# Kernel tuning notes

Measured on AMD Instinct MI355X. Metric: run time of the kernel, lower is better.

Reference implementation:

```python
import jax, jax.numpy as jnp
import numpy as np

K = 16  # number of neighbors (self excluded), matches init k
NUM_CLASSES = 100


def setup_inputs() -> dict:
    key = jax.random.key(0)
    kx, ky = jax.random.split(key)
    N, D = 8192, 256
    x = jax.random.normal(kx, (N, D), dtype=jnp.float32)
    y = jax.random.randint(ky, (N,), 0, NUM_CLASSES, dtype=jnp.int64)
    return {"x": x, "y": y}


def _knn_loss(x, y):
    N = x.shape[0]
    k = min(K, N - 1)
    # Pairwise squared Euclidean distances via Gram trick: [N, N]
    sq_norms = jnp.sum(x * x, axis=1)
    sq = sq_norms[:, None] + sq_norms[None, :] - 2.0 * (x @ x.T)
    sq = jnp.maximum(sq, 0.0)
    eye = jnp.eye(N, dtype=bool)
    # Keep sqrt grad-safe on the (excluded) diagonal by placing a dummy 1.0 there.
    d = jnp.sqrt(jnp.where(eye, 1.0, sq))  # [N, N] Euclidean distances

    # k nearest neighbors excluding self (BallTree query k+1 then drop col 0).
    d_for_knn = jnp.where(eye, jnp.inf, d)
    _, nn_idx = jax.lax.top_k(-d_for_knn, k)  # [N, k] indices of smallest distances

    # distances = exp(-d); denominator sums over all j != i.
    exp_d = jnp.where(eye, 0.0, jnp.exp(-d))
    denom = jnp.sum(exp_d, axis=1)  # [N]

    # log(exp(-d_in) / denom_i) = -d_in - log(denom_i)
    nn_d = jnp.take_along_axis(d, nn_idx, axis=1)          # [N, k]
    log_p = -nn_d - jnp.log(denom)[:, None]                 # [N, k]

    # Only neighbors with matching label contribute; rows with none are skipped.
    match = (y[nn_idx] == y[:, None]).astype(x.dtype)       # [N, k]
    cnt = jnp.sum(match, axis=1)                            # [N]
    row_mean = jnp.where(cnt > 0, jnp.sum(log_p * match, axis=1) / jnp.maximum(cnt, 1.0), 0.0)
    return -jnp.sum(row_mean) / N


def reference(x, y):
    return _knn_loss(x, y)
```

## Files before the change

kernel.cpp:

```cpp
#include <hip/hip_runtime.h>
#include <hip/hip_fp16.h>


typedef __attribute__((ext_vector_type(8))) short s8v;
typedef __attribute__((ext_vector_type(4))) float f32x4;

#define NK 256

template <bool B> struct BoolC { static constexpr bool value = B; };

#define OFF_NRM 0
#define OFF_XB  32768

__device__ __forceinline__ unsigned short f2bf(float f) {
  unsigned u = __float_as_uint(f);
  return (unsigned short)((u + 0x7FFFu + ((u >> 16) & 1u)) >> 16);
}

__device__ __forceinline__ unsigned umin32(unsigned a, unsigned b) { return a < b ? a : b; }
__device__ __forceinline__ unsigned umax32(unsigned a, unsigned b) { return a > b ? a : b; }

__global__ __launch_bounds__(256) void k_prep(const float* __restrict__ x,
                                              unsigned short* __restrict__ xb,
                                              float* __restrict__ nrm,
                                              float* __restrict__ out) {
  if (blockIdx.x == 0 && threadIdx.x == 0) out[0] = 0.0f;
  const int w = threadIdx.x >> 6, l = threadIdx.x & 63;
  const int r = blockIdx.x * 4 + w;
  const float4 xv = *reinterpret_cast<const float4*>(x + r * NK + l * 4);
  float ns = xv.x * xv.x + xv.y * xv.y + xv.z * xv.z + xv.w * xv.w;
  ns += __shfl_xor(ns, 1);  ns += __shfl_xor(ns, 2);  ns += __shfl_xor(ns, 4);
  ns += __shfl_xor(ns, 8);  ns += __shfl_xor(ns, 16); ns += __shfl_xor(ns, 32);
  if (l == 0) nrm[r] = ns;
  ushort4 bv;
  bv.x = f2bf(xv.x); bv.y = f2bf(xv.y); bv.z = f2bf(xv.z); bv.w = f2bf(xv.w);
  const int gs = (l >> 1) ^ (r & 7);
  *reinterpret_cast<ushort4*>(xb + r * NK + gs * 8 + (l & 1) * 4) = bv;
}

__global__ __launch_bounds__(512, 2) void k_mega(const unsigned short* __restrict__ xb,
                                                 const float* __restrict__ nrm,
                                                 const int* __restrict__ y,
                                                 float* __restrict__ out) {
  __shared__ float ncsAll[8192];
  __shared__ float dpart[32];
  __shared__ unsigned cl[32][256];
  const int tid = threadIdx.x;
  const int w = tid >> 6, l = tid & 63, l15 = l & 15, l4 = l >> 4;
  const int rb = blockIdx.x;
  const int rowbase = rb * 32;

  #pragma unroll
  for (int j = 0; j < 16; ++j) ncsAll[tid + j * 512] = nrm[tid + j * 512];
  if (tid < 32) dpart[tid] = 0.0f;

  s8v A[2][8];
  #pragma unroll
  for (int rf = 0; rf < 2; ++rf) {
    const int rr = rowbase + rf * 16 + l15;
    #pragma unroll
    for (int kf = 0; kf < 8; ++kf) {
      const int g = ((kf << 2) | l4) ^ (rr & 7);
      A[rf][kf] = *reinterpret_cast<const s8v*>(xb + rr * NK + g * 8);
    }
  }
  float nr[2][4], dn[2][4];
  unsigned s0[2][4], s1[2][4];
  #pragma unroll
  for (int rf = 0; rf < 2; ++rf)
    #pragma unroll
    for (int q = 0; q < 4; ++q) {
      nr[rf][q] = nrm[rowbase + rf * 16 + l4 * 4 + q];
      dn[rf][q] = 0.0f;
      s0[rf][q] = 0xFFFFFFFFu;
      s1[rf][q] = 0xFFFFFFFFu;
    }

  int koff[8];
  #pragma unroll
  for (int kf = 0; kf < 8; ++kf)
    koff[kf] = ((((kf << 2) | l4) ^ (l15 & 7)) << 4);
  const char* xbc = (const char*)xb;
  const int tdg = rb >> 1;

  __syncthreads();

  for (int i = 0; i < 16; ++i) {
    const int t = w + i * 8;
    const int cbase = t * 64;
    const char* bp = xbc + (size_t)(cbase + l15) * 512;
    f32x4 acc[2][4];
    #pragma unroll
    for (int cf = 0; cf < 4; ++cf) {
      f32x4 z = {0.f, 0.f, 0.f, 0.f};
      acc[0][cf] = z; acc[1][cf] = z;
    }
    #pragma unroll
    for (int kf = 0; kf < 8; ++kf) {
      const s8v b0 = *reinterpret_cast<const s8v*>(bp + koff[kf]);
      const s8v b1 = *reinterpret_cast<const s8v*>(bp + 8192 + koff[kf]);
      const s8v b2 = *reinterpret_cast<const s8v*>(bp + 16384 + koff[kf]);
      const s8v b3 = *reinterpret_cast<const s8v*>(bp + 24576 + koff[kf]);
      acc[0][0] = __builtin_amdgcn_mfma_f32_16x16x32_bf16(A[0][kf], b0, acc[0][0], 0, 0, 0);
      acc[1][0] = __builtin_amdgcn_mfma_f32_16x16x32_bf16(A[1][kf], b0, acc[1][0], 0, 0, 0);
      acc[0][1] = __builtin_amdgcn_mfma_f32_16x16x32_bf16(A[0][kf], b1, acc[0][1], 0, 0, 0);
      acc[1][1] = __builtin_amdgcn_mfma_f32_16x16x32_bf16(A[1][kf], b1, acc[1][1], 0, 0, 0);
      acc[0][2] = __builtin_amdgcn_mfma_f32_16x16x32_bf16(A[0][kf], b2, acc[0][2], 0, 0, 0);
      acc[1][2] = __builtin_amdgcn_mfma_f32_16x16x32_bf16(A[1][kf], b2, acc[1][2], 0, 0, 0);
      acc[0][3] = __builtin_amdgcn_mfma_f32_16x16x32_bf16(A[0][kf], b3, acc[0][3], 0, 0, 0);
      acc[1][3] = __builtin_amdgcn_mfma_f32_16x16x32_bf16(A[1][kf], b3, acc[1][3], 0, 0, 0);
    }
    float nc[4];
    #pragma unroll
    for (int cf = 0; cf < 4; ++cf) nc[cf] = ncsAll[cbase + cf * 16 + l15];
    auto epi = [&](auto dgc) {
      constexpr bool DG = decltype(dgc)::value;
      #pragma unroll
      for (int rf = 0; rf < 2; ++rf)
        #pragma unroll
        for (int cf = 0; cf < 4; ++cf) {
          const unsigned colg = (unsigned)(cbase + cf * 16 + l15);
          #pragma unroll
          for (int q = 0; q < 4; ++q) {
            const unsigned rowg = (unsigned)(rowbase + rf * 16 + l4 * 4 + q);
            float sq = fmaf(acc[rf][cf][q], -2.0f, nr[rf][q] + nc[cf]);
            if (DG) sq = fmaxf(sq, 0.0f);
            const float d = __builtin_amdgcn_sqrtf(sq);
            float e = __expf(-d);
            unsigned k = ((unsigned)__half_as_ushort(__float2half(d)) << 16) | colg;
            if (DG) {
              const bool nd = (rowg != colg);
              e = nd ? e : 0.0f;
              k = nd ? k : 0xFFFFFFFFu;
            }
            dn[rf][q] += e;
            const unsigned ev = umax32(s0[rf][q], k);
            s0[rf][q] = umin32(s0[rf][q], k);
            s1[rf][q] = umin32(s1[rf][q], ev);
          }
        }
    };
    if (t == tdg) epi(BoolC<true>{});
    else          epi(BoolC<false>{});
  }

  #pragma unroll
  for (int rf = 0; rf < 2; ++rf)
    #pragma unroll
    for (int q = 0; q < 4; ++q) {
      float vs = dn[rf][q];
      vs += __shfl_xor(vs, 1); vs += __shfl_xor(vs, 2);
      vs += __shfl_xor(vs, 4); vs += __shfl_xor(vs, 8);
      const int row32 = rf * 16 + l4 * 4 + q;
      if (l15 == 0) atomicAdd(&dpart[row32], vs);
      cl[row32][w * 32 + l15 * 2]     = s0[rf][q];
      cl[row32][w * 32 + l15 * 2 + 1] = s1[rf][q];
    }
  __syncthreads();

  float wsum = 0.0f;
  for (int rr = 0; rr < 4; ++rr) {
    const int row = w * 4 + rr;
    unsigned kk[4];
    #pragma unroll
    for (int j = 0; j < 4; ++j) kk[j] = cl[row][l * 4 + j];
    unsigned myKey = 0xFFFFFFFFu;
    for (int pp = 0; pp < 16; ++pp) {
      const unsigned lm = umin32(umin32(kk[0], kk[1]), umin32(kk[2], kk[3]));
      unsigned m = lm;
      m = umin32(m, __shfl_xor(m, 1));  m = umin32(m, __shfl_xor(m, 2));
      m = umin32(m, __shfl_xor(m, 4));  m = umin32(m, __shfl_xor(m, 8));
      m = umin32(m, __shfl_xor(m, 16)); m = umin32(m, __shfl_xor(m, 32));
      const unsigned long long bal = __ballot(lm == m);
      const int owner = (int)__ffsll(bal) - 1;
      if (l == owner) {
        bool f = false;
        #pragma unroll
        for (int j = 0; j < 4; ++j)
          if (!f && kk[j] == m) { kk[j] = 0xFFFFFFFFu; f = true; }
      }
      if (l == pp) myKey = m;
    }
    const float logden = __logf(dpart[row]);
    float contrib = 0.0f, cmf = 0.0f;
    if (l < 16 && myKey != 0xFFFFFFFFu) {
      const int col = (int)(myKey & 0x1FFFu);
      const float dd = __half2float(__ushort_as_half((unsigned short)(myKey >> 16)));
      if (y[col] == y[rowbase + row]) { contrib = -dd - logden; cmf = 1.0f; }
    }
    contrib += __shfl_xor(contrib, 1);  contrib += __shfl_xor(contrib, 2);
    contrib += __shfl_xor(contrib, 4);  contrib += __shfl_xor(contrib, 8);
    contrib += __shfl_xor(contrib, 16); contrib += __shfl_xor(contrib, 32);
    cmf += __shfl_xor(cmf, 1);  cmf += __shfl_xor(cmf, 2);
    cmf += __shfl_xor(cmf, 4);  cmf += __shfl_xor(cmf, 8);
    cmf += __shfl_xor(cmf, 16); cmf += __shfl_xor(cmf, 32);
    if (cmf > 0.0f) wsum += contrib / cmf;
  }
  if (l == 0) atomicAdd(out, wsum * (-1.0f / 8192.0f));
}

extern "C" void kernel_launch(void* const* d_in, const int* in_sizes, int n_in,
                              void* d_out, int out_size, void* d_ws, size_t ws_size,
                              hipStream_t stream) {
  const float* x = (const float*)d_in[0];
  const int* y = (const int*)d_in[1];
  float* out = (float*)d_out;
  char* ws = (char*)d_ws;

  float*          nrm = (float*)(ws + OFF_NRM);
  unsigned short* xb  = (unsigned short*)(ws + OFF_XB);

  k_prep<<<2048, 256, 0, stream>>>(x, xb, nrm, out);
  k_mega<<<256,  512, 0, stream>>>(xb, nrm, y, out);
}
```

Baseline: 110.7 us.

## Split column range across two blocks per row tile and merge top-k in a finalize kernel

The main kernel now splits the 8192 columns into two halves, so 512 blocks run instead of 256, each with half the shared norm buffer and a higher occupancy hint. Each block writes its per-row partial top-16 keys and partial denominators to workspace, and a new finalize kernel merges the two candidate lists per row, sums the denominators and computes the loss. This is meant to fill more of the GPU's compute units with the 256-block grid, at the cost of an extra launch and a global-memory round trip for the partial results.

```diff
diff --git a/kernel.cpp b/kernel.cpp
--- a/kernel.cpp
+++ b/kernel.cpp
@@ -11,6 +11,8 @@
 
 #define OFF_NRM 0
 #define OFF_XB  32768
+#define OFF_TOP (32768 + 4194304)
+#define OFF_DNP (OFF_TOP + 1048576)
 
 __device__ __forceinline__ unsigned short f2bf(float f) {
   unsigned u = __float_as_uint(f);
@@ -38,20 +40,21 @@
   *reinterpret_cast<ushort4*>(xb + r * NK + gs * 8 + (l & 1) * 4) = bv;
 }
 
-__global__ __launch_bounds__(512, 2) void k_mega(const unsigned short* __restrict__ xb,
+__global__ __launch_bounds__(512, 4) void k_mega(const unsigned short* __restrict__ xb,
                                                  const float* __restrict__ nrm,
-                                                 const int* __restrict__ y,
-                                                 float* __restrict__ out) {
-  __shared__ float ncsAll[8192];
+                                                 unsigned* __restrict__ top16g,
+                                                 float* __restrict__ dnpg) {
+  __shared__ float ncsAll[4096];
   __shared__ float dpart[32];
   __shared__ unsigned cl[32][256];
   const int tid = threadIdx.x;
   const int w = tid >> 6, l = tid & 63, l15 = l & 15, l4 = l >> 4;
-  const int rb = blockIdx.x;
+  const int rb = blockIdx.x >> 1, cs = blockIdx.x & 1;
   const int rowbase = rb * 32;
-
-  #pragma unroll
-  for (int j = 0; j < 16; ++j) ncsAll[tid + j * 512] = nrm[tid + j * 512];
+  const int colbase = cs * 4096;
+
+  #pragma unroll
+  for (int j = 0; j < 8; ++j) ncsAll[tid + j * 512] = nrm[colbase + tid + j * 512];
   if (tid < 32) dpart[tid] = 0.0f;
 
   s8v A[2][8];
@@ -85,8 +88,9 @@
 
   __syncthreads();
 
-  for (int i = 0; i < 16; ++i) {
-    const int t = w + i * 8;
+  for (int i = 0; i < 8; ++i) {
+    const int tl = w + i * 8;
+    const int t = cs * 64 + tl;
     const int cbase = t * 64;
     const char* bp = xbc + (size_t)(cbase + l15) * 512;
     f32x4 acc[2][4];
@@ -112,7 +116,7 @@
     }
     float nc[4];
     #pragma unroll
-    for (int cf = 0; cf < 4; ++cf) nc[cf] = ncsAll[cbase + cf * 16 + l15];
+    for (int cf = 0; cf < 4; ++cf) nc[cf] = ncsAll[tl * 64 + cf * 16 + l15];
     auto epi = [&](auto dgc) {
       constexpr bool DG = decltype(dgc)::value;
       #pragma unroll
@@ -158,7 +162,6 @@
     }
   __syncthreads();
 
-  float wsum = 0.0f;
   for (int rr = 0; rr < 4; ++rr) {
     const int row = w * 4 + rr;
     unsigned kk[4];
@@ -181,22 +184,46 @@
       }
       if (l == pp) myKey = m;
     }
-    const float logden = __logf(dpart[row]);
-    float contrib = 0.0f, cmf = 0.0f;
-    if (l < 16 && myKey != 0xFFFFFFFFu) {
-      const int col = (int)(myKey & 0x1FFFu);
-      const float dd = __half2float(__ushort_as_half((unsigned short)(myKey >> 16)));
-      if (y[col] == y[rowbase + row]) { contrib = -dd - logden; cmf = 1.0f; }
-    }
-    contrib += __shfl_xor(contrib, 1);  contrib += __shfl_xor(contrib, 2);
-    contrib += __shfl_xor(contrib, 4);  contrib += __shfl_xor(contrib, 8);
-    contrib += __shfl_xor(contrib, 16); contrib += __shfl_xor(contrib, 32);
-    cmf += __shfl_xor(cmf, 1);  cmf += __shfl_xor(cmf, 2);
-    cmf += __shfl_xor(cmf, 4);  cmf += __shfl_xor(cmf, 8);
-    cmf += __shfl_xor(cmf, 16); cmf += __shfl_xor(cmf, 32);
-    if (cmf > 0.0f) wsum += contrib / cmf;
-  }
-  if (l == 0) atomicAdd(out, wsum * (-1.0f / 8192.0f));
+    const int rowg = rowbase + row;
+    if (l < 16) top16g[(rowg * 2 + cs) * 16 + l] = myKey;
+    if (l == 16) dnpg[rowg * 2 + cs] = dpart[row];
+  }
+}
+
+__global__ __launch_bounds__(256) void k_fin(const unsigned* __restrict__ top16g,
+                                             const float* __restrict__ dnpg,
+                                             const int* __restrict__ y,
+                                             float* __restrict__ out) {
+  const int w = threadIdx.x >> 6, l = threadIdx.x & 63;
+  const int r = blockIdx.x * 4 + w;
+  unsigned kk = (l < 32) ? top16g[r * 32 + l] : 0xFFFFFFFFu;
+  unsigned myKey = 0xFFFFFFFFu;
+  for (int pp = 0; pp < 16; ++pp) {
+    unsigned m = kk;
+    m = umin32(m, __shfl_xor(m, 1));  m = umin32(m, __shfl_xor(m, 2));
+    m = umin32(m, __shfl_xor(m, 4));  m = umin32(m, __shfl_xor(m, 8));
+    m = umin32(m, __shfl_xor(m, 16)); m = umin32(m, __shfl_xor(m, 32));
+    const unsigned long long bal = __ballot(kk == m);
+    const int owner = (int)__ffsll(bal) - 1;
+    if (l == owner) kk = 0xFFFFFFFFu;
+    if (l == pp) myKey = m;
+  }
+  const float den = dnpg[r * 2] + dnpg[r * 2 + 1];
+  const float logden = __logf(den);
+  float contrib = 0.0f, cmf = 0.0f;
+  if (l < 16 && myKey != 0xFFFFFFFFu) {
+    const int col = (int)(myKey & 0x1FFFu);
+    const float dd = __half2float(__ushort_as_half((unsigned short)(myKey >> 16)));
+    if (y[col] == y[r]) { contrib = -dd - logden; cmf = 1.0f; }
+  }
+  contrib += __shfl_xor(contrib, 1);  contrib += __shfl_xor(contrib, 2);
+  contrib += __shfl_xor(contrib, 4);  contrib += __shfl_xor(contrib, 8);
+  contrib += __shfl_xor(contrib, 16); contrib += __shfl_xor(contrib, 32);
+  cmf += __shfl_xor(cmf, 1);  cmf += __shfl_xor(cmf, 2);
+  cmf += __shfl_xor(cmf, 4);  cmf += __shfl_xor(cmf, 8);
+  cmf += __shfl_xor(cmf, 16); cmf += __shfl_xor(cmf, 32);
+  if (l == 0 && cmf > 0.0f)
+    atomicAdd(out, (contrib / cmf) * (-1.0f / 8192.0f));
 }
 
 extern "C" void kernel_launch(void* const* d_in, const int* in_sizes, int n_in,
@@ -207,9 +234,12 @@
   float* out = (float*)d_out;
   char* ws = (char*)d_ws;
 
-  float*          nrm = (float*)(ws + OFF_NRM);
-  unsigned short* xb  = (unsigned short*)(ws + OFF_XB);
+  float*          nrm    = (float*)(ws + OFF_NRM);
+  unsigned short* xb     = (unsigned short*)(ws + OFF_XB);
+  unsigned*       top16g = (unsigned*)(ws + OFF_TOP);
+  float*          dnpg   = (float*)(ws + OFF_DNP);
 
   k_prep<<<2048, 256, 0, stream>>>(x, xb, nrm, out);
-  k_mega<<<256,  512, 0, stream>>>(xb, nrm, y, out);
-}
+  k_mega<<<512,  512, 0, stream>>>(xb, nrm, top16g, dnpg);
+  k_fin <<<2048, 256, 0, stream>>>(top16g, dnpg, y, out);
+}
```

Result: slower. 174.8 us (+57.9%).
